# Kernel optimization log

Hardware: AMD Instinct MI355X
Metric: run time of the kernel (lower is better)

## Reference

```python
import jax, jax.numpy as jnp
import numpy as np

N, E, F, H, C, ED = 10000, 160000, 4, 32, 4, 2  # nodes, edges, in_feat, hidden, classes, edge_dim


def _init(key, shape, fan_in):
    return jax.random.normal(key, shape, jnp.float32) / np.float32(np.sqrt(fan_in))


def setup_inputs() -> dict:
    key = jax.random.key(0)
    ks = iter(jax.random.split(key, 40))
    inp = {
        "x": jax.random.normal(next(ks), (N, F), jnp.float32),
        "edge_index": jax.random.randint(next(ks), (2, E), 0, N, dtype=jnp.int32),
        "edge_attr": jax.random.normal(next(ks), (E, ED), jnp.float32),
    }
    for i, din in enumerate([F, H, H]):
        inp[f"w1_{i}"] = _init(next(ks), (ED, H), ED)
        inp[f"b1_{i}"] = jnp.zeros((H,), jnp.float32)
        inp[f"w2_{i}"] = _init(next(ks), (H, din * H), H)
        inp[f"b2_{i}"] = jnp.zeros((din * H,), jnp.float32)
        inp[f"root_{i}"] = _init(next(ks), (din, H), din)
        inp[f"bias_{i}"] = jnp.zeros((H,), jnp.float32)
    inp["fc_w"] = _init(next(ks), (H, C), H)
    inp["fc_b"] = jnp.zeros((C,), jnp.float32)
    return inp


def _nnconv(x, src, dst, edge_attr, w1, b1, w2, b2, root, bias):
    # edge MLP -> per-edge weight matrix [E, din, H]
    h = jax.nn.relu(edge_attr @ w1 + b1)                      # [E, H]
    W = (h @ w2 + b2).reshape(E, x.shape[1], -1)              # [E, din, H]
    msg = jnp.einsum('ei,eio->eo', x[src], W)                 # gather + per-edge matvec
    agg = jax.ops.segment_sum(msg, dst, num_segments=N)       # scatter-add to targets
    return agg + x @ root + bias                              # root weight + bias (NNConv)


def reference(x, edge_index, edge_attr,
              w1_0, b1_0, w2_0, b2_0, root_0, bias_0,
              w1_1, b1_1, w2_1, b2_1, root_1, bias_1,
              w1_2, b1_2, w2_2, b2_2, root_2, bias_2,
              fc_w, fc_b):
    src, dst = edge_index[0], edge_index[1]
    layers = [(w1_0, b1_0, w2_0, b2_0, root_0, bias_0),
              (w1_1, b1_1, w2_1, b2_1, root_1, bias_1),
              (w1_2, b1_2, w2_2, b2_2, root_2, bias_2)]
    for p in layers:
        x = jax.nn.relu(_nnconv(x, src, dst, edge_attr, *p))  # dropout=0 -> no-op
    logits = x @ fc_w + fc_b
    return jax.nn.log_softmax(logits, axis=1)
```

## Files before the change

kernel.cpp:

```cpp
#include <hip/hip_runtime.h>
#include <hip/hip_bf16.h>
#include <math.h>

#define N_NODES 10000
#define N_EDGES 160000

typedef __attribute__((ext_vector_type(8))) short bf16x8;
typedef __attribute__((ext_vector_type(4))) float f32x4;
typedef __attribute__((ext_vector_type(4))) double f64x4;

static __device__ inline unsigned short f2b(float v) {
    __hip_bfloat16 b = __float2bfloat16(v);
    return *reinterpret_cast<unsigned short*>(&b);
}
static __device__ inline float b2f(unsigned short u) {
    union { unsigned int i; float f; } c;
    c.i = ((unsigned int)u) << 16;
    return c.f;
}

__global__ __launch_bounds__(256) void k_tw2z(const float* __restrict__ s0,
                                              const float* __restrict__ s1,
                                              const float* __restrict__ s2,
                                              float* __restrict__ t0,
                                              float* __restrict__ t1,
                                              float* __restrict__ t2,
                                              int* __restrict__ cntz) {
    int tid = blockIdx.x * 256 + threadIdx.x;
    if (tid < 20480) { cntz[tid] = 0; return; }
    int d = tid - 20480;
    if (d < 4096) {
        int i = d >> 10, j = d & 1023, o = j >> 5, k = j & 31;
        t0[d] = s0[k * 128 + i * 32 + o];
    } else if (d < 4096 + 32768) {
        int q = d - 4096;
        int i = q >> 10, j = q & 1023, o = j >> 5, k = j & 31;
        t1[q] = s1[k * 1024 + i * 32 + o];
    } else if (d < 4096 + 65536) {
        int q = d - 4096 - 32768;
        int i = q >> 10, j = q & 1023, o = j >> 5, k = j & 31;
        t2[q] = s2[k * 1024 + i * 32 + o];
    }
}

__global__ __launch_bounds__(256) void k_hist2(const int* __restrict__ ei,
                                               int* __restrict__ cnt,
                                               int* __restrict__ cntd) {
    int e = blockIdx.x * 256 + threadIdx.x;
    if (e < N_EDGES) {
        atomicAdd(&cnt[ei[e]], 1);
        atomicAdd(&cntd[ei[N_EDGES + e]], 1);
    }
}

__global__ __launch_bounds__(256) void k_scan2(const int* __restrict__ cnt,
                                               const int* __restrict__ cntd,
                                               int* __restrict__ off,
                                               int* __restrict__ dst_off,
                                               int* __restrict__ cursor,
                                               int* __restrict__ cursord) {
    const int* c; int* o; int* cu;
    if (blockIdx.x == 0) { c = cnt;  o = off;     cu = cursor;  }
    else                 { c = cntd; o = dst_off; cu = cursord; }
    __shared__ int part[256];
    int t = threadIdx.x;
    int base = t * 40;
    int s = 0;
    for (int i = 0; i < 40; ++i) {
        int idx = base + i;
        if (idx < N_NODES) s += c[idx];
    }
    part[t] = s;
    __syncthreads();
    for (int d = 1; d < 256; d <<= 1) {
        int v = (t >= d) ? part[t - d] : 0;
        __syncthreads();
        part[t] += v;
        __syncthreads();
    }
    int run = part[t] - s;
    for (int i = 0; i < 40; ++i) {
        int idx = base + i;
        if (idx < N_NODES) {
            o[idx] = run;
            cu[idx] = run;
            run += c[idx];
        }
    }
    if (t == 255) o[N_NODES] = run;
}

__global__ __launch_bounds__(256) void k_scatter(const int* __restrict__ ei,
                                                 const float* __restrict__ ea,
                                                 int* __restrict__ cursor,
                                                 int* __restrict__ cursord,
                                                 int* __restrict__ qmap,
                                                 float* __restrict__ ea_s) {
    int e = blockIdx.x * 256 + threadIdx.x;
    if (e >= N_EDGES) return;
    float a0 = ea[2 * e], a1 = ea[2 * e + 1];
    int src = ei[e], dst = ei[N_EDGES + e];
    int pos = atomicAdd(&cursor[src], 1);
    int q   = atomicAdd(&cursord[dst], 1);
    qmap[pos] = q;
    *(float2*)(ea_s + 2 * (size_t)pos) = make_float2(a0, a1);
}

template <int DIN, bool FIRST>
__global__ __launch_bounds__(256) void k_G(const float* __restrict__ xin,
                                           const int* __restrict__ dst_off,
                                           const unsigned short* __restrict__ msgd,
                                           const float* __restrict__ w2t,
                                           const float* __restrict__ b2,
                                           const float* __restrict__ root,
                                           const float* __restrict__ bias,
                                           unsigned short* __restrict__ Gb,
                                           float* __restrict__ xb2,
                                           float* __restrict__ agg) {
    const int t = threadIdx.x;
    const int n0 = blockIdx.x * 8;

    __shared__ float xs[8 * DIN];
    if constexpr (FIRST) {
        for (int idx = t; idx < 8 * DIN; idx += 256) {
            int m = idx / DIN, i = idx - m * DIN;
            xs[idx] = xin[(size_t)(n0 + m) * DIN + i];
        }
        __syncthreads();
    } else {
        __shared__ f64x4 part[256];
        {
            int m = t >> 5, s = t & 31;
            int g = s >> 2, quar = s & 3;
            int n = n0 + m;
            int jb = dst_off[n], je = dst_off[n + 1];
            f64x4 a0 = {0.0, 0.0, 0.0, 0.0}, a1 = {0.0, 0.0, 0.0, 0.0};
            int j = jb + quar;
            for (; j + 4 < je; j += 8) {
                ushort4 u0 = *(const ushort4*)(msgd + (size_t)j * 32 + g * 4);
                ushort4 u1 = *(const ushort4*)(msgd + (size_t)(j + 4) * 32 + g * 4);
                a0[0] += (double)b2f(u0.x); a0[1] += (double)b2f(u0.y);
                a0[2] += (double)b2f(u0.z); a0[3] += (double)b2f(u0.w);
                a1[0] += (double)b2f(u1.x); a1[1] += (double)b2f(u1.y);
                a1[2] += (double)b2f(u1.z); a1[3] += (double)b2f(u1.w);
            }
            if (j < je) {
                ushort4 u0 = *(const ushort4*)(msgd + (size_t)j * 32 + g * 4);
                a0[0] += (double)b2f(u0.x); a0[1] += (double)b2f(u0.y);
                a0[2] += (double)b2f(u0.z); a0[3] += (double)b2f(u0.w);
            }
            part[t] = a0 + a1;
        }
        __syncthreads();
        if (t < 64) {
            int m = t >> 3, g = t & 7;
            f64x4 v = part[m * 32 + g * 4] + part[m * 32 + g * 4 + 1] +
                      part[m * 32 + g * 4 + 2] + part[m * 32 + g * 4 + 3];
            int n = n0 + m;
            float2 xiA = *(const float2*)(xin + (size_t)n * 32 + 2 * g);
            float2 xiB = *(const float2*)(xin + (size_t)n * 32 + 16 + 2 * g);
            float r0 = (float)(v[0] + (double)xiA.x);
            float r2 = (float)(v[2] + (double)xiA.y);
            float r1 = (float)(v[1] + (double)xiB.x);
            float r3 = (float)(v[3] + (double)xiB.y);
            xs[m * 32 + 2 * g]      = r0 > 0.f ? r0 : 0.f;
            xs[m * 32 + 2 * g + 1]  = r2 > 0.f ? r2 : 0.f;
            xs[m * 32 + 2 * g + 16] = r1 > 0.f ? r1 : 0.f;
            xs[m * 32 + 2 * g + 17] = r3 > 0.f ? r3 : 0.f;
        }
        __syncthreads();
    }

    float acc[8][4];
#pragma unroll
    for (int m = 0; m < 8; ++m)
        acc[m][0] = acc[m][1] = acc[m][2] = acc[m][3] = 0.f;

#pragma unroll
    for (int i = 0; i < DIN; ++i) {
        const float4 w = *(const float4*)(w2t + i * 1024 + t * 4);
#pragma unroll
        for (int m = 0; m < 8; ++m) {
            float xv = xs[m * DIN + i];
            acc[m][0] += xv * w.x;
            acc[m][1] += xv * w.y;
            acc[m][2] += xv * w.z;
            acc[m][3] += xv * w.w;
        }
    }
#pragma unroll
    for (int m = 0; m < 8; ++m) {
        unsigned int p0 = (unsigned int)f2b(acc[m][0]) | ((unsigned int)f2b(acc[m][1]) << 16);
        unsigned int p1 = (unsigned int)f2b(acc[m][2]) | ((unsigned int)f2b(acc[m][3]) << 16);
        *(uint2*)(Gb + (size_t)(n0 + m) * 1024 + t * 4) = make_uint2(p0, p1);
    }

    {
        int m = t >> 5, o = t & 31;
        float ab = 0.f, ar = bias[o];
#pragma unroll
        for (int i = 0; i < DIN; ++i) {
            float xv = xs[m * DIN + i];
            ab += xv * b2[i * 32 + o];
            ar += xv * root[i * 32 + o];
        }
        size_t p = (size_t)(n0 + m) * 32 + o;
        xb2[p] = ab;
        agg[p] = ar;
    }
}

__global__ __launch_bounds__(256) void k_edge(const int* __restrict__ off,
                                              const int* __restrict__ qmap,
                                              const float* __restrict__ ea_s,
                                              const float* __restrict__ w1,
                                              const float* __restrict__ b1,
                                              const unsigned short* __restrict__ Gb,
                                              const float* __restrict__ xb2,
                                              unsigned short* __restrict__ msgd) {
    int t = threadIdx.x;
    int lane = t & 63;
    int n = blockIdx.x * 4 + (t >> 6);
    int col = lane & 15;
    int quad = lane >> 4;

    float wa[8], wb[8], bb[8];
#pragma unroll
    for (int j = 0; j < 8; ++j) {
        int o = quad * 8 + j;
        wa[j] = w1[o];
        wb[j] = w1[32 + o];
        bb[j] = b1[o];
    }

    const bf16x8 b_lo = *(const bf16x8*)(Gb + (size_t)n * 1024 + col * 32 + quad * 8);
    const bf16x8 b_hi = *(const bf16x8*)(Gb + (size_t)n * 1024 + (col + 16) * 32 + quad * 8);
    float xb_lo = xb2[(size_t)n * 32 + col];
    float xb_hi = xb2[(size_t)n * 32 + 16 + col];

    int jb = off[n], je = off[n + 1];
    for (int e0 = jb; e0 < je; e0 += 16) {
        int eA = e0 + col;
        bf16x8 afrag = {0, 0, 0, 0, 0, 0, 0, 0};
        if (eA < je) {
            float2 a = *(const float2*)(ea_s + 2 * (size_t)eA);
            union { unsigned int u[4]; bf16x8 v; } cv;
#pragma unroll
            for (int j = 0; j < 4; ++j) {
                float v0 = fmaxf(a.x * wa[2 * j]     + a.y * wb[2 * j]     + bb[2 * j],     0.f);
                float v1 = fmaxf(a.x * wa[2 * j + 1] + a.y * wb[2 * j + 1] + bb[2 * j + 1], 0.f);
                cv.u[j] = (unsigned int)f2b(v0) | ((unsigned int)f2b(v1) << 16);
            }
            afrag = cv.v;
        }
        f32x4 acc_lo = {xb_lo, xb_lo, xb_lo, xb_lo};
        f32x4 acc_hi = {xb_hi, xb_hi, xb_hi, xb_hi};
        acc_lo = __builtin_amdgcn_mfma_f32_16x16x32_bf16(afrag, b_lo, acc_lo, 0, 0, 0);
        acc_hi = __builtin_amdgcn_mfma_f32_16x16x32_bf16(afrag, b_hi, acc_hi, 0, 0, 0);
#pragma unroll
        for (int r = 0; r < 4; ++r) {
            int er = e0 + quad * 4 + r;
            if (er < je) {
                int q = qmap[er];
                unsigned int pk = (unsigned int)f2b(acc_lo[r]) |
                                  ((unsigned int)f2b(acc_hi[r]) << 16);
                *(unsigned int*)(msgd + (size_t)q * 32 + col * 2) = pk;
            }
        }
    }
}

__global__ __launch_bounds__(256) void k_final(const float* __restrict__ agg,
                                               const int* __restrict__ dst_off,
                                               const unsigned short* __restrict__ msgd,
                                               const float* __restrict__ fcw,
                                               const float* __restrict__ fcb,
                                               float* __restrict__ out) {
    __shared__ f64x4 part[256];
    __shared__ float xs[8 * 32];
    int t = threadIdx.x;
    {
        int m = t >> 5, s = t & 31;
        int g = s >> 2, quar = s & 3;
        int n = blockIdx.x * 8 + m;
        int jb = dst_off[n], je = dst_off[n + 1];
        f64x4 a0 = {0.0, 0.0, 0.0, 0.0}, a1 = {0.0, 0.0, 0.0, 0.0};
        int j = jb + quar;
        for (; j + 4 < je; j += 8) {
            ushort4 u0 = *(const ushort4*)(msgd + (size_t)j * 32 + g * 4);
            ushort4 u1 = *(const ushort4*)(msgd + (size_t)(j + 4) * 32 + g * 4);
            a0[0] += (double)b2f(u0.x); a0[1] += (double)b2f(u0.y);
            a0[2] += (double)b2f(u0.z); a0[3] += (double)b2f(u0.w);
            a1[0] += (double)b2f(u1.x); a1[1] += (double)b2f(u1.y);
            a1[2] += (double)b2f(u1.z); a1[3] += (double)b2f(u1.w);
        }
        if (j < je) {
            ushort4 u0 = *(const ushort4*)(msgd + (size_t)j * 32 + g * 4);
            a0[0] += (double)b2f(u0.x); a0[1] += (double)b2f(u0.y);
            a0[2] += (double)b2f(u0.z); a0[3] += (double)b2f(u0.w);
        }
        part[t] = a0 + a1;
    }
    __syncthreads();
    if (t < 64) {
        int m = t >> 3, g = t & 7;
        f64x4 v = part[m * 32 + g * 4] + part[m * 32 + g * 4 + 1] +
                  part[m * 32 + g * 4 + 2] + part[m * 32 + g * 4 + 3];
        int n = blockIdx.x * 8 + m;
        float2 agA = *(const float2*)(agg + (size_t)n * 32 + 2 * g);
        float2 agB = *(const float2*)(agg + (size_t)n * 32 + 16 + 2 * g);
        float r0 = (float)(v[0] + (double)agA.x);
        float r2 = (float)(v[2] + (double)agA.y);
        float r1 = (float)(v[1] + (double)agB.x);
        float r3 = (float)(v[3] + (double)agB.y);
        xs[m * 32 + 2 * g]      = r0 > 0.f ? r0 : 0.f;
        xs[m * 32 + 2 * g + 1]  = r2 > 0.f ? r2 : 0.f;
        xs[m * 32 + 2 * g + 16] = r1 > 0.f ? r1 : 0.f;
        xs[m * 32 + 2 * g + 17] = r3 > 0.f ? r3 : 0.f;
    }
    __syncthreads();
    if (t < 8) {
        int nn = blockIdx.x * 8 + t;
        float l0 = fcb[0], l1 = fcb[1], l2 = fcb[2], l3 = fcb[3];
#pragma unroll
        for (int oo = 0; oo < 32; ++oo) {
            float xv = xs[t * 32 + oo];
            l0 += xv * fcw[oo * 4 + 0];
            l1 += xv * fcw[oo * 4 + 1];
            l2 += xv * fcw[oo * 4 + 2];
            l3 += xv * fcw[oo * 4 + 3];
        }
        float mx = fmaxf(fmaxf(l0, l1), fmaxf(l2, l3));
        float s = expf(l0 - mx) + expf(l1 - mx) + expf(l2 - mx) + expf(l3 - mx);
        float lse = mx + logf(s);
        out[(size_t)nn * 4 + 0] = l0 - lse;
        out[(size_t)nn * 4 + 1] = l1 - lse;
        out[(size_t)nn * 4 + 2] = l2 - lse;
        out[(size_t)nn * 4 + 3] = l3 - lse;
    }
}

extern "C" void kernel_launch(void* const* d_in, const int* in_sizes, int n_in,
                              void* d_out, int out_size, void* d_ws, size_t ws_size,
                              hipStream_t stream) {
    const float* x0 = (const float*)d_in[0];
    const int*   ei = (const int*)d_in[1];
    const float* ea = (const float*)d_in[2];
    const float *W1[3], *B1[3], *W2[3], *B2[3], *RT[3], *BS[3];
    for (int l = 0; l < 3; ++l) {
        W1[l] = (const float*)d_in[3 + 6 * l];
        B1[l] = (const float*)d_in[4 + 6 * l];
        W2[l] = (const float*)d_in[5 + 6 * l];
        B2[l] = (const float*)d_in[6 + 6 * l];
        RT[l] = (const float*)d_in[7 + 6 * l];
        BS[l] = (const float*)d_in[8 + 6 * l];
    }
    const float* fcw = (const float*)d_in[21];
    const float* fcb = (const float*)d_in[22];
    float* out = (float*)d_out;

    int*   cnt     = (int*)d_ws;
    int*   cntd    = cnt + 10240;
    int*   cursor  = cntd + 10240;
    int*   cursord = cursor + 10240;
    int*   off     = cursord + 10240;
    int*   dst_off = off + 10240;
    int*   qmap    = dst_off + 10240;
    float* w2t0    = (float*)(qmap + 160000);
    float* w2t1    = w2t0 + 4096;
    float* w2t2    = w2t1 + 32768;
    float* xb2     = w2t2 + 32768;
    float* aggA    = xb2 + 320000;
    float* aggB    = aggA + 320000;
    unsigned short* msgd = (unsigned short*)(aggB + 320000);
    float* ea_s    = (float*)(msgd + 5120000);
    unsigned short* Gb = (unsigned short*)(ea_s + 320000);

    const int gE256 = (N_EDGES + 255) / 256;
    const int gG    = N_NODES / 8;
    const int gEdge = N_NODES / 4;

    k_tw2z<<<352, 256, 0, stream>>>(W2[0], W2[1], W2[2], w2t0, w2t1, w2t2, cnt);
    k_hist2<<<gE256, 256, 0, stream>>>(ei, cnt, cntd);
    k_scan2<<<2, 256, 0, stream>>>(cnt, cntd, off, dst_off, cursor, cursord);
    k_scatter<<<gE256, 256, 0, stream>>>(ei, ea, cursor, cursord, qmap, ea_s);

    k_G<4, true><<<gG, 256, 0, stream>>>(x0, dst_off, msgd, w2t0, B2[0], RT[0], BS[0], Gb, xb2, aggA);
    k_edge<<<gEdge, 256, 0, stream>>>(off, qmap, ea_s, W1[0], B1[0], Gb, xb2, msgd);

    k_G<32, false><<<gG, 256, 0, stream>>>(aggA, dst_off, msgd, w2t1, B2[1], RT[1], BS[1], Gb, xb2, aggB);
    k_edge<<<gEdge, 256, 0, stream>>>(off, qmap, ea_s, W1[1], B1[1], Gb, xb2, msgd);

    k_G<32, false><<<gG, 256, 0, stream>>>(aggB, dst_off, msgd, w2t2, B2[2], RT[2], BS[2], Gb, xb2, aggA);
    k_edge<<<gEdge, 256, 0, stream>>>(off, qmap, ea_s, W1[2], B1[2], Gb, xb2, msgd);

    k_final<<<(N_NODES + 7) / 8, 256, 0, stream>>>(aggA, dst_off, msgd, fcw, fcb, out);
}
```

Before: 251.8 us.

## Fuse per-node weight build and edge message kernels into one per-layer kernel

Merges k_G and k_edge into a single kernel per layer. Each block builds the bf16 per-node weight matrices for 8 nodes and then processes those nodes' outgoing edges after a block barrier, so Gb and xb2 are read back right after being written, likely from cache. Message buffers are double-buffered (msgdA/msgdB), because a layer's edge phase scatters messages that other blocks in the same launch may still be reading from the previous layer. This removes three kernel launches and the global round trip between the two stages. In exchange, edge work is now split 2 nodes per wave instead of 1, which may cause load imbalance, and the workspace grows by one extra message buffer.

Result: faster. 244.5 us (-2.9%).

```diff
diff --git a/kernel.cpp b/kernel.cpp
--- a/kernel.cpp
+++ b/kernel.cpp
@@ -107,16 +107,22 @@
 }
 
 template <int DIN, bool FIRST>
-__global__ __launch_bounds__(256) void k_G(const float* __restrict__ xin,
-                                           const int* __restrict__ dst_off,
-                                           const unsigned short* __restrict__ msgd,
-                                           const float* __restrict__ w2t,
-                                           const float* __restrict__ b2,
-                                           const float* __restrict__ root,
-                                           const float* __restrict__ bias,
-                                           unsigned short* __restrict__ Gb,
-                                           float* __restrict__ xb2,
-                                           float* __restrict__ agg) {
+__global__ __launch_bounds__(256) void k_GE(const float* __restrict__ xin,
+                                            const int* __restrict__ dst_off,
+                                            const unsigned short* __restrict__ msgd_in,
+                                            const float* __restrict__ w2t,
+                                            const float* __restrict__ b2,
+                                            const float* __restrict__ root,
+                                            const float* __restrict__ bias,
+                                            const int* __restrict__ off,
+                                            const int* __restrict__ qmap,
+                                            const float* __restrict__ ea_s,
+                                            const float* __restrict__ w1,
+                                            const float* __restrict__ b1,
+                                            unsigned short* __restrict__ Gb,
+                                            float* __restrict__ xb2,
+                                            float* __restrict__ agg,
+                                            unsigned short* __restrict__ msgd_out) {
     const int t = threadIdx.x;
     const int n0 = blockIdx.x * 8;
 
@@ -137,15 +143,15 @@
             f64x4 a0 = {0.0, 0.0, 0.0, 0.0}, a1 = {0.0, 0.0, 0.0, 0.0};
             int j = jb + quar;
             for (; j + 4 < je; j += 8) {
-                ushort4 u0 = *(const ushort4*)(msgd + (size_t)j * 32 + g * 4);
-                ushort4 u1 = *(const ushort4*)(msgd + (size_t)(j + 4) * 32 + g * 4);
+                ushort4 u0 = *(const ushort4*)(msgd_in + (size_t)j * 32 + g * 4);
+                ushort4 u1 = *(const ushort4*)(msgd_in + (size_t)(j + 4) * 32 + g * 4);
                 a0[0] += (double)b2f(u0.x); a0[1] += (double)b2f(u0.y);
                 a0[2] += (double)b2f(u0.z); a0[3] += (double)b2f(u0.w);
                 a1[0] += (double)b2f(u1.x); a1[1] += (double)b2f(u1.y);
                 a1[2] += (double)b2f(u1.z); a1[3] += (double)b2f(u1.w);
             }
             if (j < je) {
-                ushort4 u0 = *(const ushort4*)(msgd + (size_t)j * 32 + g * 4);
+                ushort4 u0 = *(const ushort4*)(msgd_in + (size_t)j * 32 + g * 4);
                 a0[0] += (double)b2f(u0.x); a0[1] += (double)b2f(u0.y);
                 a0[2] += (double)b2f(u0.z); a0[3] += (double)b2f(u0.w);
             }
@@ -171,100 +177,98 @@
         __syncthreads();
     }
 
-    float acc[8][4];
-#pragma unroll
-    for (int m = 0; m < 8; ++m)
-        acc[m][0] = acc[m][1] = acc[m][2] = acc[m][3] = 0.f;
-
-#pragma unroll
-    for (int i = 0; i < DIN; ++i) {
-        const float4 w = *(const float4*)(w2t + i * 1024 + t * 4);
+    {
+        float acc[8][4];
+#pragma unroll
+        for (int m = 0; m < 8; ++m)
+            acc[m][0] = acc[m][1] = acc[m][2] = acc[m][3] = 0.f;
+
+#pragma unroll
+        for (int i = 0; i < DIN; ++i) {
+            const float4 w = *(const float4*)(w2t + i * 1024 + t * 4);
+#pragma unroll
+            for (int m = 0; m < 8; ++m) {
+                float xv = xs[m * DIN + i];
+                acc[m][0] += xv * w.x;
+                acc[m][1] += xv * w.y;
+                acc[m][2] += xv * w.z;
+                acc[m][3] += xv * w.w;
+            }
+        }
 #pragma unroll
         for (int m = 0; m < 8; ++m) {
-            float xv = xs[m * DIN + i];
-            acc[m][0] += xv * w.x;
-            acc[m][1] += xv * w.y;
-            acc[m][2] += xv * w.z;
-            acc[m][3] += xv * w.w;
-        }
-    }
-#pragma unroll
-    for (int m = 0; m < 8; ++m) {
-        unsigned int p0 = (unsigned int)f2b(acc[m][0]) | ((unsigned int)f2b(acc[m][1]) << 16);
-        unsigned int p1 = (unsigned int)f2b(acc[m][2]) | ((unsigned int)f2b(acc[m][3]) << 16);
-        *(uint2*)(Gb + (size_t)(n0 + m) * 1024 + t * 4) = make_uint2(p0, p1);
-    }
+            unsigned int p0 = (unsigned int)f2b(acc[m][0]) | ((unsigned int)f2b(acc[m][1]) << 16);
+            unsigned int p1 = (unsigned int)f2b(acc[m][2]) | ((unsigned int)f2b(acc[m][3]) << 16);
+            *(uint2*)(Gb + (size_t)(n0 + m) * 1024 + t * 4) = make_uint2(p0, p1);
+        }
+
+        {
+            int m = t >> 5, o = t & 31;
+            float ab = 0.f, ar = bias[o];
+#pragma unroll
+            for (int i = 0; i < DIN; ++i) {
+                float xv = xs[m * DIN + i];
+                ab += xv * b2[i * 32 + o];
+                ar += xv * root[i * 32 + o];
+            }
+            size_t p = (size_t)(n0 + m) * 32 + o;
+            xb2[p] = ab;
+            agg[p] = ar;
+        }
+    }
+
+    __syncthreads();
 
     {
-        int m = t >> 5, o = t & 31;
-        float ab = 0.f, ar = bias[o];
-#pragma unroll
-        for (int i = 0; i < DIN; ++i) {
-            float xv = xs[m * DIN + i];
-            ab += xv * b2[i * 32 + o];
-            ar += xv * root[i * 32 + o];
-        }
-        size_t p = (size_t)(n0 + m) * 32 + o;
-        xb2[p] = ab;
-        agg[p] = ar;
-    }
-}
-
-__global__ __launch_bounds__(256) void k_edge(const int* __restrict__ off,
-                                              const int* __restrict__ qmap,
-                                              const float* __restrict__ ea_s,
-                                              const float* __restrict__ w1,
-                                              const float* __restrict__ b1,
-                                              const unsigned short* __restrict__ Gb,
-                                              const float* __restrict__ xb2,
-                                              unsigned short* __restrict__ msgd) {
-    int t = threadIdx.x;
-    int lane = t & 63;
-    int n = blockIdx.x * 4 + (t >> 6);
-    int col = lane & 15;
-    int quad = lane >> 4;
-
-    float wa[8], wb[8], bb[8];
-#pragma unroll
-    for (int j = 0; j < 8; ++j) {
-        int o = quad * 8 + j;
-        wa[j] = w1[o];
-        wb[j] = w1[32 + o];
-        bb[j] = b1[o];
-    }
-
-    const bf16x8 b_lo = *(const bf16x8*)(Gb + (size_t)n * 1024 + col * 32 + quad * 8);
-    const bf16x8 b_hi = *(const bf16x8*)(Gb + (size_t)n * 1024 + (col + 16) * 32 + quad * 8);
-    float xb_lo = xb2[(size_t)n * 32 + col];
-    float xb_hi = xb2[(size_t)n * 32 + 16 + col];
-
-    int jb = off[n], je = off[n + 1];
-    for (int e0 = jb; e0 < je; e0 += 16) {
-        int eA = e0 + col;
-        bf16x8 afrag = {0, 0, 0, 0, 0, 0, 0, 0};
-        if (eA < je) {
-            float2 a = *(const float2*)(ea_s + 2 * (size_t)eA);
-            union { unsigned int u[4]; bf16x8 v; } cv;
-#pragma unroll
-            for (int j = 0; j < 4; ++j) {
-                float v0 = fmaxf(a.x * wa[2 * j]     + a.y * wb[2 * j]     + bb[2 * j],     0.f);
-                float v1 = fmaxf(a.x * wa[2 * j + 1] + a.y * wb[2 * j + 1] + bb[2 * j + 1], 0.f);
-                cv.u[j] = (unsigned int)f2b(v0) | ((unsigned int)f2b(v1) << 16);
-            }
-            afrag = cv.v;
-        }
-        f32x4 acc_lo = {xb_lo, xb_lo, xb_lo, xb_lo};
-        f32x4 acc_hi = {xb_hi, xb_hi, xb_hi, xb_hi};
-        acc_lo = __builtin_amdgcn_mfma_f32_16x16x32_bf16(afrag, b_lo, acc_lo, 0, 0, 0);
-        acc_hi = __builtin_amdgcn_mfma_f32_16x16x32_bf16(afrag, b_hi, acc_hi, 0, 0, 0);
-#pragma unroll
-        for (int r = 0; r < 4; ++r) {
-            int er = e0 + quad * 4 + r;
-            if (er < je) {
-                int q = qmap[er];
-                unsigned int pk = (unsigned int)f2b(acc_lo[r]) |
-                                  ((unsigned int)f2b(acc_hi[r]) << 16);
-                *(unsigned int*)(msgd + (size_t)q * 32 + col * 2) = pk;
+        int lane = t & 63, wave = t >> 6;
+        int col = lane & 15;
+        int quad = lane >> 4;
+
+        float wa[8], wb[8], bb[8];
+#pragma unroll
+        for (int j = 0; j < 8; ++j) {
+            int o = quad * 8 + j;
+            wa[j] = w1[o];
+            wb[j] = w1[32 + o];
+            bb[j] = b1[o];
+        }
+
+        for (int nn = 0; nn < 2; ++nn) {
+            int n = n0 + wave * 2 + nn;
+            const bf16x8 b_lo = *(const bf16x8*)(Gb + (size_t)n * 1024 + col * 32 + quad * 8);
+            const bf16x8 b_hi = *(const bf16x8*)(Gb + (size_t)n * 1024 + (col + 16) * 32 + quad * 8);
+            float xb_lo = xb2[(size_t)n * 32 + col];
+            float xb_hi = xb2[(size_t)n * 32 + 16 + col];
+
+            int jb = off[n], je = off[n + 1];
+            for (int e0 = jb; e0 < je; e0 += 16) {
+                int eA = e0 + col;
+                bf16x8 afrag = {0, 0, 0, 0, 0, 0, 0, 0};
+                if (eA < je) {
+                    float2 a = *(const float2*)(ea_s + 2 * (size_t)eA);
+                    union { unsigned int u[4]; bf16x8 v; } cv;
+#pragma unroll
+                    for (int j = 0; j < 4; ++j) {
+                        float v0 = fmaxf(a.x * wa[2 * j]     + a.y * wb[2 * j]     + bb[2 * j],     0.f);
+                        float v1 = fmaxf(a.x * wa[2 * j + 1] + a.y * wb[2 * j + 1] + bb[2 * j + 1], 0.f);
+                        cv.u[j] = (unsigned int)f2b(v0) | ((unsigned int)f2b(v1) << 16);
+                    }
+                    afrag = cv.v;
+                }
+                f32x4 acc_lo = {xb_lo, xb_lo, xb_lo, xb_lo};
+                f32x4 acc_hi = {xb_hi, xb_hi, xb_hi, xb_hi};
+                acc_lo = __builtin_amdgcn_mfma_f32_16x16x32_bf16(afrag, b_lo, acc_lo, 0, 0, 0);
+                acc_hi = __builtin_amdgcn_mfma_f32_16x16x32_bf16(afrag, b_hi, acc_hi, 0, 0, 0);
+#pragma unroll
+                for (int r = 0; r < 4; ++r) {
+                    int er = e0 + quad * 4 + r;
+                    if (er < je) {
+                        int q = qmap[er];
+                        unsigned int pk = (unsigned int)f2b(acc_lo[r]) |
+                                          ((unsigned int)f2b(acc_hi[r]) << 16);
+                        *(unsigned int*)(msgd_out + (size_t)q * 32 + col * 2) = pk;
+                    }
+                }
             }
         }
     }
@@ -372,27 +376,25 @@
     float* xb2     = w2t2 + 32768;
     float* aggA    = xb2 + 320000;
     float* aggB    = aggA + 320000;
-    unsigned short* msgd = (unsigned short*)(aggB + 320000);
-    float* ea_s    = (float*)(msgd + 5120000);
+    unsigned short* msgdA = (unsigned short*)(aggB + 320000);
+    unsigned short* msgdB = msgdA + 5120000;
+    float* ea_s    = (float*)(msgdB + 5120000);
     unsigned short* Gb = (unsigned short*)(ea_s + 320000);
 
     const int gE256 = (N_EDGES + 255) / 256;
-    const int gG    = N_NODES / 8;
-    const int gEdge = N_NODES / 4;
+    const int gL    = N_NODES / 8;
 
     k_tw2z<<<352, 256, 0, stream>>>(W2[0], W2[1], W2[2], w2t0, w2t1, w2t2, cnt);
     k_hist2<<<gE256, 256, 0, stream>>>(ei, cnt, cntd);
     k_scan2<<<2, 256, 0, stream>>>(cnt, cntd, off, dst_off, cursor, cursord);
     k_scatter<<<gE256, 256, 0, stream>>>(ei, ea, cursor, cursord, qmap, ea_s);
 
-    k_G<4, true><<<gG, 256, 0, stream>>>(x0, dst_off, msgd, w2t0, B2[0], RT[0], BS[0], Gb, xb2, aggA);
-    k_edge<<<gEdge, 256, 0, stream>>>(off, qmap, ea_s, W1[0], B1[0], Gb, xb2, msgd);
-
-    k_G<32, false><<<gG, 256, 0, stream>>>(aggA, dst_off, msgd, w2t1, B2[1], RT[1], BS[1], Gb, xb2, aggB);
-    k_edge<<<gEdge, 256, 0, stream>>>(off, qmap, ea_s, W1[1], B1[1], Gb, xb2, msgd);
-
-    k_G<32, false><<<gG, 256, 0, stream>>>(aggB, dst_off, msgd, w2t2, B2[2], RT[2], BS[2], Gb, xb2, aggA);
-    k_edge<<<gEdge, 256, 0, stream>>>(off, qmap, ea_s, W1[2], B1[2], Gb, xb2, msgd);
-
-    k_final<<<(N_NODES + 7) / 8, 256, 0, stream>>>(aggA, dst_off, msgd, fcw, fcb, out);
-}
+    k_GE<4, true><<<gL, 256, 0, stream>>>(x0, dst_off, msgdB , w2t0, B2[0], RT[0], BS[0],
+                                          off, qmap, ea_s, W1[0], B1[0], Gb, xb2, aggA, msgdA);
+    k_GE<32, false><<<gL, 256, 0, stream>>>(aggA, dst_off, msgdA, w2t1, B2[1], RT[1], BS[1],
+                                            off, qmap, ea_s, W1[1], B1[1], Gb, xb2, aggB, msgdB);
+    k_GE<32, false><<<gL, 256, 0, stream>>>(aggB, dst_off, msgdB, w2t2, B2[2], RT[2], BS[2],
+                                            off, qmap, ea_s, W1[2], B1[2], Gb, xb2, aggA, msgdA);
+
+    k_final<<<gL, 256, 0, stream>>>(aggA, dst_off, msgdA, fcw, fcb, out);
+}
```
